# Kernel tuning notes

Hardware: AMD Instinct MI355X
Metric: run time of the kernel (lower is better)

The kernel has to match this reference:

```python
import jax, jax.numpy as jnp
import numpy as np

N_SRC = 50000
N_DST = 50000
E = 800000
D = 128
K = 8  # args.k: number of randomly sampled neighbors


def setup_inputs() -> dict:
    key = jax.random.key(0)
    k1, k2, k3, k4, k5, k6 = jax.random.split(key, 6)
    h_src = jax.random.normal(k1, (N_SRC, D), dtype=jnp.float32)
    h_dst = jax.random.normal(k2, (N_DST, D), dtype=jnp.float32)
    unif = jax.random.uniform(k3, (N_DST, K), dtype=jnp.float32)
    src_idx = jax.random.randint(k4, (E,), 0, N_SRC, dtype=jnp.int32)
    dst_idx = jnp.sort(jax.random.randint(k5, (E,), 0, N_DST, dtype=jnp.int32))
    category = jax.random.randint(k6, (N_SRC,), 0, 50, dtype=jnp.int32)
    return {"h_src": h_src, "h_dst": h_dst, "unif": unif,
            "src_idx": src_idx, "dst_idx": dst_idx, "category": category}


def _forward(h_src, h_dst, unif, src_idx, dst_idx, category):
    n_src = h_src.shape[0]
    n_dst = h_dst.shape[0]
    e = src_idx.shape[0]
    ones = jnp.ones((e,), dtype=h_src.dtype)

    # src-side symmetric norm: feat_src * out_deg^-0.5
    out_deg = jax.ops.segment_sum(ones, src_idx, num_segments=n_src)
    out_norm = jnp.clip(out_deg, 1.0, None) ** -0.5
    feat_src = h_src * out_norm[:, None]

    # mailbox gather: message per edge m_e = feat_src[src_e]  -> [E, D]
    msg = feat_src[src_idx]

    # in-degrees and full segment-sum reduction
    in_deg = jax.ops.segment_sum(ones, dst_idx, num_segments=n_dst)
    full_sum = jax.ops.segment_sum(msg, dst_idx, num_segments=n_dst)  # [N_dst, D]

    # random neighbor subsampling with replacement (dst_idx is sorted):
    # node n owns edges [ptr[n], ptr[n]+deg[n]); pick K offsets via floor(u*deg)
    deg_i = in_deg.astype(jnp.int32)
    ptr = jnp.searchsorted(dst_idx, jnp.arange(n_dst, dtype=jnp.int32), side="left").astype(jnp.int32)
    off = jnp.floor(unif * in_deg[:, None]).astype(jnp.int32)
    off = jnp.minimum(off, jnp.maximum(deg_i[:, None] - 1, 0))  # guard u==1 / deg==0
    eid = jnp.clip(ptr[:, None] + off, 0, e - 1)                # [N_dst, K]
    samp_sum = msg[eid].sum(axis=1)                              # [N_dst, D]

    # bucket escape hatch: any incoming category == -1 -> sum everything
    neg_in = jax.ops.segment_sum((category[src_idx] == -1).astype(jnp.int32),
                                 dst_idx, num_segments=n_dst)
    use_full = (deg_i <= K) | (neg_in > 0)
    rst = jnp.where(use_full[:, None], full_sum, samp_sum)

    # dst-side norm: rst * in_deg^-0.5
    in_norm = jnp.clip(in_deg, 1.0, None) ** -0.5
    return rst * in_norm[:, None]


def reference(h_src, h_dst, unif, src_idx, dst_idx, category):
    return _forward(h_src, h_dst, unif, src_idx, dst_idx, category)
```

## Files before the change

### kernel.cpp

```cpp
#include <hip/hip_runtime.h>

#define N_SRC 50000
#define N_DST 50000
#define E_CNT 800000
#define D 128
#define K 8

#define HIST_BLOCKS 64
#define HIST_THREADS 512
#define PTR_BLOCKS ((N_DST + 1 + HIST_THREADS - 1) / HIST_THREADS)
#define HALF 25000
#define HWORDS (HALF / 2)
#define NCHUNK (E_CNT / 4)


__global__ __launch_bounds__(HIST_THREADS)
void count_ptr_kernel(const int* __restrict__ src_idx,
                      const int* __restrict__ dst_idx,
                      const int* __restrict__ category,
                      int* __restrict__ slab,
                      int* __restrict__ neg_in,
                      int* __restrict__ ptr) {
    if (blockIdx.x < HIST_BLOCKS) {
        __shared__ int hist[HWORDS];
        const int4* s4 = (const int4*)src_idx;
        int* myslab = slab + (size_t)blockIdx.x * N_SRC;

        for (int pass = 0; pass < 2; ++pass) {
            int base = pass * HALF;
            for (int j = threadIdx.x; j < HWORDS; j += HIST_THREADS) hist[j] = 0;
            __syncthreads();

            for (int c = blockIdx.x * HIST_THREADS + threadIdx.x; c < NCHUNK;
                 c += HIST_BLOCKS * HIST_THREADS) {
                int4 s = s4[c];
                int r;
                r = s.x - base; if ((unsigned)r < HALF) atomicAdd(&hist[r >> 1], 1 << ((r & 1) * 16));
                r = s.y - base; if ((unsigned)r < HALF) atomicAdd(&hist[r >> 1], 1 << ((r & 1) * 16));
                r = s.z - base; if ((unsigned)r < HALF) atomicAdd(&hist[r >> 1], 1 << ((r & 1) * 16));
                r = s.w - base; if ((unsigned)r < HALF) atomicAdd(&hist[r >> 1], 1 << ((r & 1) * 16));
                if (pass == 0) {
                    if (category[s.x] == -1) atomicAdd(&neg_in[dst_idx[4 * c + 0]], 1);
                    if (category[s.y] == -1) atomicAdd(&neg_in[dst_idx[4 * c + 1]], 1);
                    if (category[s.z] == -1) atomicAdd(&neg_in[dst_idx[4 * c + 2]], 1);
                    if (category[s.w] == -1) atomicAdd(&neg_in[dst_idx[4 * c + 3]], 1);
                }
            }
            __syncthreads();

            for (int j = threadIdx.x; j < HWORDS; j += HIST_THREADS) {
                unsigned w = (unsigned)hist[j];
                ((int2*)(myslab + base))[j] = make_int2((int)(w & 0xffffu), (int)(w >> 16));
            }
            __syncthreads();
        }
    } else {
        int n = (blockIdx.x - HIST_BLOCKS) * HIST_THREADS + threadIdx.x;
        if (n > N_DST) return;
        int lo = 0, hi = E_CNT;
        while (lo < hi) {
            int mid = (lo + hi) >> 1;
            if (dst_idx[mid] < n) lo = mid + 1; else hi = mid;
        }
        ptr[n] = lo;
    }
}

__global__ void reduce_norm_kernel(const int* __restrict__ slab,
                                   float* __restrict__ out_norm) {
    int n = blockIdx.x * blockDim.x + threadIdx.x;
    if (n >= N_SRC) return;
    int d = 0;
    #pragma unroll
    for (int b = 0; b < HIST_BLOCKS; ++b) d += slab[(size_t)b * N_SRC + n];
    out_norm[n] = rsqrtf((float)max(d, 1));
}

__global__ void gather_kernel(const float* __restrict__ h_src,
                              const float* __restrict__ unif,
                              const int* __restrict__ src_idx,
                              const float* __restrict__ out_norm,
                              const int* __restrict__ neg_in,
                              const int* __restrict__ ptr,
                              float* __restrict__ out) {
    int wave = (blockIdx.x * blockDim.x + threadIdx.x) >> 6;
    int lane = threadIdx.x & 63;
    int sub = lane & 31;
    int n = wave * 2 + (lane >> 5);
    if (n >= N_DST) return;

    int p = ptr[n];
    int deg = ptr[n + 1] - p;
    bool use_full = (deg <= K) || (neg_in[n] > 0);

    const float4* h4 = (const float4*)h_src;
    float4 acc = make_float4(0.f, 0.f, 0.f, 0.f);

    if (use_full) {
        for (int i = 0; i < deg; ++i) {
            int s = src_idx[p + i];
            float norm = out_norm[s];
            float4 v = h4[(size_t)s * 32 + sub];
            acc.x += v.x * norm;
            acc.y += v.y * norm;
            acc.z += v.z * norm;
            acc.w += v.w * norm;
        }
    } else {
        int s_k = 0;
        if (sub < K) {
            float u = unif[n * K + sub];
            int off = (int)floorf(u * (float)deg);
            if (off > deg - 1) off = deg - 1;
            if (off < 0) off = 0;
            int eid = p + off;
            if (eid < 0) eid = 0;
            if (eid > E_CNT - 1) eid = E_CNT - 1;
            s_k = src_idx[eid];
        }
        #pragma unroll
        for (int k = 0; k < K; ++k) {
            int s = __shfl(s_k, (lane & 32) + k, 64);
            float norm = out_norm[s];
            float4 v = h4[(size_t)s * 32 + sub];
            acc.x += v.x * norm;
            acc.y += v.y * norm;
            acc.z += v.z * norm;
            acc.w += v.w * norm;
        }
    }

    float in_norm = rsqrtf((float)max(deg, 1));
    float4 r;
    r.x = acc.x * in_norm;
    r.y = acc.y * in_norm;
    r.z = acc.z * in_norm;
    r.w = acc.w * in_norm;
    ((float4*)out)[(size_t)n * 32 + sub] = r;
}

extern "C" void kernel_launch(void* const* d_in, const int* in_sizes, int n_in,
                              void* d_out, int out_size, void* d_ws, size_t ws_size,
                              hipStream_t stream) {
    const float* h_src   = (const float*)d_in[0];
    const float* unif    = (const float*)d_in[2];
    const int* src_idx   = (const int*)d_in[3];
    const int* dst_idx   = (const int*)d_in[4];
    const int* category  = (const int*)d_in[5];
    float* out = (float*)d_out;

    int* slab      = (int*)d_ws;
    int* neg_in    = slab + (size_t)HIST_BLOCKS * N_SRC;
    int* ptr       = neg_in + N_DST;
    float* out_norm = (float*)(ptr + N_DST + 1);

    hipMemsetAsync(neg_in, 0, (size_t)N_DST * sizeof(int), stream);

    count_ptr_kernel<<<HIST_BLOCKS + PTR_BLOCKS, HIST_THREADS, 0, stream>>>(
        src_idx, dst_idx, category, slab, neg_in, ptr);

    reduce_norm_kernel<<<(N_SRC + 255) / 256, 256, 0, stream>>>(slab, out_norm);

    {
        int threads = 256;
        int blocks = (N_DST + 7) / 8;
        gather_kernel<<<blocks, threads, 0, stream>>>(h_src, unif, src_idx,
                                                      out_norm, neg_in,
                                                      ptr, out);
    }
}
```

Baseline: 142.9 us.

## Prescale source features into bf16 buffer and gather half-width rows

Replaces the norm-reduction kernel with a kernel that computes the source out-degree norm, multiplies it into h_src, and stores the result as packed bf16. The gather then reads 256-byte bf16 rows instead of 512-byte fp32 rows and no longer does a per-edge norm lookup. Lane mapping changes to 16 lanes per node, 4 nodes per wave. This cuts random-gather traffic, but it adds an extra pass over h_src and introduces bf16 rounding error relative to the fp32 reference.

```diff
diff --git a/kernel.cpp b/kernel.cpp
--- a/kernel.cpp
+++ b/kernel.cpp
@@ -66,45 +66,78 @@
     }
 }
 
-__global__ void reduce_norm_kernel(const int* __restrict__ slab,
-                                   float* __restrict__ out_norm) {
-    int n = blockIdx.x * blockDim.x + threadIdx.x;
-    if (n >= N_SRC) return;
-    int d = 0;
-    #pragma unroll
-    for (int b = 0; b < HIST_BLOCKS; ++b) d += slab[(size_t)b * N_SRC + n];
-    out_norm[n] = rsqrtf((float)max(d, 1));
-}
-
-__global__ void gather_kernel(const float* __restrict__ h_src,
+__device__ __forceinline__ unsigned bf16pack(float a, float b) {
+    unsigned ua = __float_as_uint(a);
+    unsigned ub = __float_as_uint(b);
+    ua = (ua + 0x7fffu + ((ua >> 16) & 1)) >> 16;
+    ub = (ub + 0x7fffu + ((ub >> 16) & 1)) & 0xffff0000u;
+    return ua | ub;
+}
+
+__global__ __launch_bounds__(256)
+void feat_kernel(const float* __restrict__ h_src,
+                 const int* __restrict__ slab,
+                 unsigned* __restrict__ feat) {
+    __shared__ float norm_lds[256];
+    int base = blockIdx.x * 256;
+    int t = threadIdx.x;
+    int n0 = base + t;
+    if (n0 < N_SRC) {
+        int d = 0;
+        #pragma unroll
+        for (int b = 0; b < HIST_BLOCKS; ++b) d += slab[(size_t)b * N_SRC + n0];
+        norm_lds[t] = rsqrtf((float)max(d, 1));
+    }
+    __syncthreads();
+
+    const float4* h4 = (const float4*)h_src;
+    uint2* f2 = (uint2*)feat;
+    for (int it = 0; it < 32; ++it) {
+        int j = it * 256 + t;
+        int nl = j >> 5;
+        int c = j & 31;
+        int n = base + nl;
+        if (n >= N_SRC) break;
+        float norm = norm_lds[nl];
+        float4 v = h4[(size_t)n * 32 + c];
+        uint2 w;
+        w.x = bf16pack(v.x * norm, v.y * norm);
+        w.y = bf16pack(v.z * norm, v.w * norm);
+        f2[(size_t)n * 32 + c] = w;
+    }
+}
+
+__global__ void gather_kernel(const unsigned* __restrict__ feat,
                               const float* __restrict__ unif,
                               const int* __restrict__ src_idx,
-                              const float* __restrict__ out_norm,
                               const int* __restrict__ neg_in,
                               const int* __restrict__ ptr,
                               float* __restrict__ out) {
     int wave = (blockIdx.x * blockDim.x + threadIdx.x) >> 6;
     int lane = threadIdx.x & 63;
-    int sub = lane & 31;
-    int n = wave * 2 + (lane >> 5);
+    int sub = lane & 15;
+    int n = wave * 4 + (lane >> 4);
     if (n >= N_DST) return;
 
     int p = ptr[n];
     int deg = ptr[n + 1] - p;
     bool use_full = (deg <= K) || (neg_in[n] > 0);
 
-    const float4* h4 = (const float4*)h_src;
-    float4 acc = make_float4(0.f, 0.f, 0.f, 0.f);
+    const uint4* f4 = (const uint4*)feat;
+    float acc[8] = {0.f, 0.f, 0.f, 0.f, 0.f, 0.f, 0.f, 0.f};
 
     if (use_full) {
         for (int i = 0; i < deg; ++i) {
             int s = src_idx[p + i];
-            float norm = out_norm[s];
-            float4 v = h4[(size_t)s * 32 + sub];
-            acc.x += v.x * norm;
-            acc.y += v.y * norm;
-            acc.z += v.z * norm;
-            acc.w += v.w * norm;
+            uint4 v = f4[(size_t)s * 16 + sub];
+            acc[0] += __uint_as_float(v.x << 16);
+            acc[1] += __uint_as_float(v.x & 0xffff0000u);
+            acc[2] += __uint_as_float(v.y << 16);
+            acc[3] += __uint_as_float(v.y & 0xffff0000u);
+            acc[4] += __uint_as_float(v.z << 16);
+            acc[5] += __uint_as_float(v.z & 0xffff0000u);
+            acc[6] += __uint_as_float(v.w << 16);
+            acc[7] += __uint_as_float(v.w & 0xffff0000u);
         }
     } else {
         int s_k = 0;
@@ -120,23 +153,27 @@
         }
         #pragma unroll
         for (int k = 0; k < K; ++k) {
-            int s = __shfl(s_k, (lane & 32) + k, 64);
-            float norm = out_norm[s];
-            float4 v = h4[(size_t)s * 32 + sub];
-            acc.x += v.x * norm;
-            acc.y += v.y * norm;
-            acc.z += v.z * norm;
-            acc.w += v.w * norm;
+            int s = __shfl(s_k, (lane & 48) + k, 64);
+            uint4 v = f4[(size_t)s * 16 + sub];
+            acc[0] += __uint_as_float(v.x << 16);
+            acc[1] += __uint_as_float(v.x & 0xffff0000u);
+            acc[2] += __uint_as_float(v.y << 16);
+            acc[3] += __uint_as_float(v.y & 0xffff0000u);
+            acc[4] += __uint_as_float(v.z << 16);
+            acc[5] += __uint_as_float(v.z & 0xffff0000u);
+            acc[6] += __uint_as_float(v.w << 16);
+            acc[7] += __uint_as_float(v.w & 0xffff0000u);
         }
     }
 
     float in_norm = rsqrtf((float)max(deg, 1));
-    float4 r;
-    r.x = acc.x * in_norm;
-    r.y = acc.y * in_norm;
-    r.z = acc.z * in_norm;
-    r.w = acc.w * in_norm;
-    ((float4*)out)[(size_t)n * 32 + sub] = r;
+    float4 r0 = make_float4(acc[0] * in_norm, acc[1] * in_norm,
+                            acc[2] * in_norm, acc[3] * in_norm);
+    float4 r1 = make_float4(acc[4] * in_norm, acc[5] * in_norm,
+                            acc[6] * in_norm, acc[7] * in_norm);
+    float4* o4 = (float4*)out;
+    o4[(size_t)n * 32 + sub * 2 + 0] = r0;
+    o4[(size_t)n * 32 + sub * 2 + 1] = r1;
 }
 
 extern "C" void kernel_launch(void* const* d_in, const int* in_sizes, int n_in,
@@ -152,20 +189,21 @@
     int* slab      = (int*)d_ws;
     int* neg_in    = slab + (size_t)HIST_BLOCKS * N_SRC;
     int* ptr       = neg_in + N_DST;
-    float* out_norm = (float*)(ptr + N_DST + 1);
+    size_t used = (size_t)HIST_BLOCKS * N_SRC + N_DST + N_DST + 1;
+    used = (used + 15) & ~(size_t)15;
+    unsigned* feat = (unsigned*)d_ws + used;
 
     hipMemsetAsync(neg_in, 0, (size_t)N_DST * sizeof(int), stream);
 
     count_ptr_kernel<<<HIST_BLOCKS + PTR_BLOCKS, HIST_THREADS, 0, stream>>>(
         src_idx, dst_idx, category, slab, neg_in, ptr);
 
-    reduce_norm_kernel<<<(N_SRC + 255) / 256, 256, 0, stream>>>(slab, out_norm);
+    feat_kernel<<<(N_SRC + 255) / 256, 256, 0, stream>>>(h_src, slab, feat);
 
     {
         int threads = 256;
-        int blocks = (N_DST + 7) / 8;
-        gather_kernel<<<blocks, threads, 0, stream>>>(h_src, unif, src_idx,
-                                                      out_norm, neg_in,
-                                                      ptr, out);
-    }
-}
+        int blocks = (N_DST + 15) / 16;
+        gather_kernel<<<blocks, threads, 0, stream>>>(feat, unif, src_idx,
+                                                      neg_in, ptr, out);
+    }
+}
```

New measurement: 151.3 us. 1.06x slower.

## Precompute sampled source ids and in-norms in the ptr phase of count kernel

Applied to the files above, without the earlier changes.

The ptr-computing blocks of the first kernel now also compute each destination's degree (via a wave shuffle of neighboring lower bounds), its in-norm, and the K sampled (or first up-to-K) source indices, and store them to workspace. The gather kernel then reads these precomputed ids, shuffles the out_norm values across lanes instead of loading them per lane, and only walks the full edge list when a negative category is present. This moves the dependent unif→src_idx load chain off the gather critical path and overlaps it with the histogram work. The cost is extra workspace traffic and more serial per-thread work in the ptr blocks.

```diff
diff --git a/kernel.cpp b/kernel.cpp
--- a/kernel.cpp
+++ b/kernel.cpp
@@ -14,13 +14,26 @@
 #define NCHUNK (E_CNT / 4)
 
 
+__device__ __forceinline__ int lower_bound_dst(const int* __restrict__ d, int key) {
+    int lo = 0, hi = E_CNT;
+    while (lo < hi) {
+        int mid = (lo + hi) >> 1;
+        if (d[mid] < key) lo = mid + 1; else hi = mid;
+    }
+    return lo;
+}
+
 __global__ __launch_bounds__(HIST_THREADS)
 void count_ptr_kernel(const int* __restrict__ src_idx,
                       const int* __restrict__ dst_idx,
                       const int* __restrict__ category,
+                      const float* __restrict__ unif,
                       int* __restrict__ slab,
                       int* __restrict__ neg_in,
-                      int* __restrict__ ptr) {
+                      int* __restrict__ ptr,
+                      float* __restrict__ in_norm,
+                      int* __restrict__ samp,
+                      unsigned char* __restrict__ degs) {
     if (blockIdx.x < HIST_BLOCKS) {
         __shared__ int hist[HWORDS];
         const int4* s4 = (const int4*)src_idx;
@@ -56,13 +69,46 @@
         }
     } else {
         int n = (blockIdx.x - HIST_BLOCKS) * HIST_THREADS + threadIdx.x;
-        if (n > N_DST) return;
-        int lo = 0, hi = E_CNT;
-        while (lo < hi) {
-            int mid = (lo + hi) >> 1;
-            if (dst_idx[mid] < n) lo = mid + 1; else hi = mid;
-        }
-        ptr[n] = lo;
+        int lane = threadIdx.x & 63;
+        int lo = 0;
+        if (n <= N_DST) {
+            lo = lower_bound_dst(dst_idx, n);
+            ptr[n] = lo;
+        }
+        int hi = __shfl_down(lo, 1, 64);
+        if (lane == 63 && n < N_DST) hi = lower_bound_dst(dst_idx, n + 1);
+        if (n >= N_DST) return;
+
+        int deg = hi - lo;
+        in_norm[n] = rsqrtf((float)max(deg, 1));
+        int m = min(deg, K);
+        degs[n] = (unsigned char)m;
+
+        int ids[K];
+        if (deg > K) {
+            const float4* u4 = (const float4*)(unif + (size_t)n * K);
+            float4 ua = u4[0], ub = u4[1];
+            float uu[K] = {ua.x, ua.y, ua.z, ua.w, ub.x, ub.y, ub.z, ub.w};
+            #pragma unroll
+            for (int k = 0; k < K; ++k) {
+                int off = (int)floorf(uu[k] * (float)deg);
+                if (off > deg - 1) off = deg - 1;
+                if (off < 0) off = 0;
+                int eid = lo + off;
+                if (eid > E_CNT - 1) eid = E_CNT - 1;
+                ids[k] = src_idx[eid];
+            }
+        } else {
+            #pragma unroll
+            for (int k = 0; k < K; ++k) {
+                int eid = lo + k;
+                if (eid > E_CNT - 1) eid = E_CNT - 1;
+                ids[k] = src_idx[eid];
+            }
+        }
+        int4* sp = (int4*)(samp + (size_t)n * K);
+        sp[0] = make_int4(ids[0], ids[1], ids[2], ids[3]);
+        sp[1] = make_int4(ids[4], ids[5], ids[6], ids[7]);
     }
 }
 
@@ -77,65 +123,63 @@
 }
 
 __global__ void gather_kernel(const float* __restrict__ h_src,
-                              const float* __restrict__ unif,
                               const int* __restrict__ src_idx,
                               const float* __restrict__ out_norm,
                               const int* __restrict__ neg_in,
                               const int* __restrict__ ptr,
+                              const float* __restrict__ in_norm,
+                              const int* __restrict__ samp,
+                              const unsigned char* __restrict__ degs,
                               float* __restrict__ out) {
     int wave = (blockIdx.x * blockDim.x + threadIdx.x) >> 6;
     int lane = threadIdx.x & 63;
     int sub = lane & 31;
+    int hbase = lane & 32;
     int n = wave * 2 + (lane >> 5);
     if (n >= N_DST) return;
 
-    int p = ptr[n];
-    int deg = ptr[n + 1] - p;
-    bool use_full = (deg <= K) || (neg_in[n] > 0);
+    int neg = neg_in[n];
+    int m = degs[n];
+    float inr = in_norm[n];
 
     const float4* h4 = (const float4*)h_src;
     float4 acc = make_float4(0.f, 0.f, 0.f, 0.f);
 
-    if (use_full) {
+    if (neg > 0) {
+        int p = ptr[n];
+        int deg = ptr[n + 1] - p;
         for (int i = 0; i < deg; ++i) {
             int s = src_idx[p + i];
-            float norm = out_norm[s];
+            float nrm = out_norm[s];
             float4 v = h4[(size_t)s * 32 + sub];
-            acc.x += v.x * norm;
-            acc.y += v.y * norm;
-            acc.z += v.z * norm;
-            acc.w += v.w * norm;
+            acc.x += v.x * nrm;
+            acc.y += v.y * nrm;
+            acc.z += v.z * nrm;
+            acc.w += v.w * nrm;
         }
     } else {
         int s_k = 0;
+        float n_k = 0.f;
         if (sub < K) {
-            float u = unif[n * K + sub];
-            int off = (int)floorf(u * (float)deg);
-            if (off > deg - 1) off = deg - 1;
-            if (off < 0) off = 0;
-            int eid = p + off;
-            if (eid < 0) eid = 0;
-            if (eid > E_CNT - 1) eid = E_CNT - 1;
-            s_k = src_idx[eid];
-        }
-        #pragma unroll
-        for (int k = 0; k < K; ++k) {
-            int s = __shfl(s_k, (lane & 32) + k, 64);
-            float norm = out_norm[s];
+            s_k = samp[(size_t)n * K + sub];
+            n_k = out_norm[s_k];
+        }
+        for (int k = 0; k < m; ++k) {
+            int s = __shfl(s_k, hbase + k, 64);
+            float nrm = __shfl(n_k, hbase + k, 64);
             float4 v = h4[(size_t)s * 32 + sub];
-            acc.x += v.x * norm;
-            acc.y += v.y * norm;
-            acc.z += v.z * norm;
-            acc.w += v.w * norm;
-        }
-    }
-
-    float in_norm = rsqrtf((float)max(deg, 1));
+            acc.x += v.x * nrm;
+            acc.y += v.y * nrm;
+            acc.z += v.z * nrm;
+            acc.w += v.w * nrm;
+        }
+    }
+
     float4 r;
-    r.x = acc.x * in_norm;
-    r.y = acc.y * in_norm;
-    r.z = acc.z * in_norm;
-    r.w = acc.w * in_norm;
+    r.x = acc.x * inr;
+    r.y = acc.y * inr;
+    r.z = acc.z * inr;
+    r.w = acc.w * inr;
     ((float4*)out)[(size_t)n * 32 + sub] = r;
 }
 
@@ -149,23 +193,27 @@
     const int* category  = (const int*)d_in[5];
     float* out = (float*)d_out;
 
-    int* slab      = (int*)d_ws;
+    int* base      = (int*)d_ws;
+    int* slab      = base;
     int* neg_in    = slab + (size_t)HIST_BLOCKS * N_SRC;
     int* ptr       = neg_in + N_DST;
-    float* out_norm = (float*)(ptr + N_DST + 1);
+    float* out_norm = (float*)(ptr + N_DST + 4);
+    float* in_norm  = out_norm + N_SRC;
+    int* samp      = (int*)(in_norm + N_DST);
+    unsigned char* degs = (unsigned char*)(samp + (size_t)N_DST * K);
 
     hipMemsetAsync(neg_in, 0, (size_t)N_DST * sizeof(int), stream);
 
     count_ptr_kernel<<<HIST_BLOCKS + PTR_BLOCKS, HIST_THREADS, 0, stream>>>(
-        src_idx, dst_idx, category, slab, neg_in, ptr);
+        src_idx, dst_idx, category, unif, slab, neg_in, ptr, in_norm, samp, degs);
 
     reduce_norm_kernel<<<(N_SRC + 255) / 256, 256, 0, stream>>>(slab, out_norm);
 
     {
         int threads = 256;
         int blocks = (N_DST + 7) / 8;
-        gather_kernel<<<blocks, threads, 0, stream>>>(h_src, unif, src_idx,
-                                                      out_norm, neg_in,
-                                                      ptr, out);
-    }
-}
+        gather_kernel<<<blocks, threads, 0, stream>>>(h_src, src_idx, out_norm,
+                                                      neg_in, ptr, in_norm,
+                                                      samp, degs, out);
+    }
+}
```

Measured after the change: 144.4 us. No clear change (+1.1%).
